# Kernel optimization log

Measured on AMD Instinct MI355X. Metric: run time of the kernel, lower is better.

Reference implementation:

```python
import jax, jax.numpy as jnp
import numpy as np

N, E = 50000, 600000
ATOM, BOND, HID, L, HEADS = 64, 16, 128, 3, 4
D = HID // HEADS  # 32


def setup_inputs() -> dict:
    key = jax.random.key(0)
    ks = jax.random.split(key, 12)
    s = lambda k, shape: (jax.random.normal(k, shape, jnp.float32) * 0.05)
    return {
        'x': jax.random.normal(ks[0], (N, ATOM), jnp.float32),
        'edge_index': jax.random.randint(ks[1], (2, E), 0, N, jnp.int32),
        'edge_attr': jax.random.normal(ks[2], (E, BOND), jnp.float32),
        'W_atom': s(ks[3], (ATOM, HID)), 'b_atom': jnp.zeros((HID,), jnp.float32),
        'W_bond': s(ks[4], (BOND, HID)), 'b_bond': jnp.zeros((HID,), jnp.float32),
        'W_lin': s(ks[5], (L, HID, HID)),      # GATConv.lin (bias-free)
        'W_edge': s(ks[6], (L, HID, HID)),     # GATConv.lin_edge (bias-free)
        'att_src': s(ks[7], (L, HEADS, D)),
        'att_dst': s(ks[8], (L, HEADS, D)),
        'att_edge': s(ks[9], (L, HEADS, D)),
        'bias_conv': jnp.zeros((L, HID), jnp.float32),
        'bn_gamma': jnp.ones((L, HID), jnp.float32),
        'bn_beta': jnp.zeros((L, HID), jnp.float32),
        'W_out': s(ks[10], (HID, HID)), 'b_out': jnp.zeros((HID,), jnp.float32),
    }


def _gat_layer(h, ea, src, dst, W, We, a_s, a_d, a_e, bias):
    n = h.shape[0]
    e = src.shape[0]
    # add_self_loops with fill_value='mean': self-loop edge_attr = mean of
    # incoming edge_attr per destination node
    loop = jnp.arange(n, dtype=src.dtype)
    deg = jax.ops.segment_sum(jnp.ones((e,), h.dtype), dst, num_segments=n)
    ea_loop = jax.ops.segment_sum(ea, dst, num_segments=n) / jnp.maximum(deg, 1.0)[:, None]
    src_f = jnp.concatenate([src, loop])
    dst_f = jnp.concatenate([dst, loop])
    ea_f = jnp.concatenate([ea, ea_loop], axis=0)   # [E+N, HID]

    xh = (h @ W).reshape(n, HEADS, D)               # [N, H, D]
    eh = (ea_f @ We).reshape(-1, HEADS, D)          # [E+N, H, D]
    a_node_src = jnp.sum(xh * a_s, axis=-1)         # [N, H]
    a_node_dst = jnp.sum(xh * a_d, axis=-1)         # [N, H]
    alpha = a_node_src[src_f] + a_node_dst[dst_f] + jnp.sum(eh * a_e, axis=-1)
    alpha = jax.nn.leaky_relu(alpha, negative_slope=0.2)  # [E+N, H]
    # softmax over incoming edges per destination (every node has a self-loop)
    amax = jax.ops.segment_max(alpha, dst_f, num_segments=n)
    expa = jnp.exp(alpha - amax[dst_f])
    den = jax.ops.segment_sum(expa, dst_f, num_segments=n)
    w = expa / (den[dst_f] + 1e-16)                 # [E+N, H]
    out = jax.ops.segment_sum(xh[src_f] * w[..., None], dst_f, num_segments=n)
    return out.reshape(n, HID) + bias


def _batch_norm(h, gamma, beta):
    mu = jnp.mean(h, axis=0)
    var = jnp.mean((h - mu) ** 2, axis=0)
    return gamma * (h - mu) * jax.lax.rsqrt(var + 1e-5) + beta


def reference(x, edge_index, edge_attr, W_atom, b_atom, W_bond, b_bond,
              W_lin, W_edge, att_src, att_dst, att_edge, bias_conv,
              bn_gamma, bn_beta, W_out, b_out):
    src, dst = edge_index[0], edge_index[1]
    h = x @ W_atom + b_atom                         # atom_embedding
    ea = edge_attr @ W_bond + b_bond                # bond_embedding (GAT path)
    for i in range(L):
        h_in = h
        h = _gat_layer(h, ea, src, dst, W_lin[i], W_edge[i],
                       att_src[i], att_dst[i], att_edge[i], bias_conv[i])
        h = _batch_norm(h, bn_gamma[i], bn_beta[i])
        h = jax.nn.relu(h)
        h = h + h_in                                # shapes always match (HID==HID)
    return h @ W_out + b_out
```

## Files before the change

### kernel.cpp

```cpp
#include <hip/hip_runtime.h>
#include <stdint.h>

#define HID 128

typedef __attribute__((ext_vector_type(8))) short bf16x8;
typedef __attribute__((ext_vector_type(4))) float f32x4;

__device__ __forceinline__ float bf2f(unsigned short u){
  union { unsigned int i; float f; } x; x.i = ((unsigned int)u) << 16; return x.f;
}
__device__ __forceinline__ unsigned short f2bf(float f){
  union { float f; unsigned int i; } x; x.f = f;
  unsigned int b = x.i;
  return (unsigned short)((b + 0x7fffu + ((b >> 16) & 1u)) >> 16);
}

struct CvList {
  const void* src[16];
  float* dst[16];
  int cnt[16];
  int n;
};
__global__ __launch_bounds__(256) void setup(CvList L, const void* x,
                                             unsigned short* xc, int n4,
                                             int* __restrict__ dflag,
                                             const int* __restrict__ ei, int E,
                                             int* __restrict__ deg){
  __shared__ int red[4];
  int tid = threadIdx.x;
  const unsigned short* xs = (const unsigned short*)x;
  unsigned short u = xs[tid];
  int ex = (u >> 7) & 0xFF;
  int v = ((((tid & 1) == 0) && u == 0) ? 1 : 0) | ((ex >= 140) ? 65536 : 0);
  #pragma unroll
  for (int m = 1; m < 64; m <<= 1) v += __shfl_xor(v, m);
  if ((tid & 63) == 0) red[tid >> 6] = v;
  __syncthreads();
  int tot = red[0] + red[1] + red[2] + red[3];
  bool isf32 = ((tot & 0xffff) >= 32) || ((tot >> 16) >= 8);
  if (blockIdx.x == 0 && tid == 0) dflag[0] = isf32 ? 1 : 0;
  int e = blockIdx.x*256 + tid;
  if (e < E) atomicAdd(&deg[ei[E + e]], 1);
  if (blockIdx.x < 256){
    for (int a = 0; a < L.n; ++a){
      const void* s = L.src[a];
      float* d = L.dst[a];
      int c = L.cnt[a];
      for (int i = blockIdx.x*256 + tid; i < c; i += 65536)
        d[i] = isf32 ? ((const float*)s)[i] : bf2f(((const unsigned short*)s)[i]);
    }
    for (int i = blockIdx.x*256 + tid; i < n4; i += 65536){
      if (isf32){
        float4 q = ((const float4*)x)[i];
        ushort4 o; o.x = f2bf(q.x); o.y = f2bf(q.y); o.z = f2bf(q.z); o.w = f2bf(q.w);
        ((ushort4*)xc)[i] = o;
      } else {
        ((ushort4*)xc)[i] = ((const ushort4*)x)[i];
      }
    }
  }
}

__global__ __launch_bounds__(256) void precompute_M(
    const float* __restrict__ We, const float* __restrict__ ae,
    const float* __restrict__ Wb, const float* __restrict__ bb,
    float* __restrict__ Mout, float* __restrict__ cb)
{
  __shared__ float ve[128*12];
  int tid = threadIdx.x;
  for (int i = tid; i < 128*12; i += 256){
    int c = i / 12, lh = i % 12; int l = lh >> 2, h = lh & 3;
    float s = 0.f;
    for (int d = 0; d < 32; ++d)
      s += We[l*16384 + c*128 + h*32 + d] * ae[l*128 + h*32 + d];
    ve[i] = s;
  }
  __syncthreads();
  for (int i = tid; i < 16*12; i += 256){
    int k = i / 12, lh = i % 12;
    float s = 0.f;
    for (int c = 0; c < 128; ++c) s += Wb[k*128 + c] * ve[c*12 + lh];
    Mout[i] = s;
  }
  for (int i = tid; i < 12; i += 256){
    float s = 0.f;
    for (int c = 0; c < 128; ++c) s += bb[c] * ve[c*12 + i];
    cb[i] = s;
  }
}

__global__ __launch_bounds__(256) void scan_part(const int* __restrict__ deg, int* __restrict__ part, int N){
  int base = blockIdx.x*1024;
  int s = 0;
  for (int i = threadIdx.x; i < 1024; i += 256){ int j = base + i; if (j < N) s += deg[j]; }
  __shared__ int sh[256];
  sh[threadIdx.x] = s; __syncthreads();
  for (int m = 128; m > 0; m >>= 1){ if (threadIdx.x < m) sh[threadIdx.x] += sh[threadIdx.x + m]; __syncthreads(); }
  if (threadIdx.x == 0) part[blockIdx.x] = sh[0];
}
__global__ void scan_top(int* part, int P){
  if (threadIdx.x == 0 && blockIdx.x == 0){
    int acc = 0;
    for (int i = 0; i < P; ++i){ int v = part[i]; part[i] = acc; acc += v; }
  }
}
__global__ __launch_bounds__(256) void scan_write(const int* __restrict__ deg, const int* __restrict__ part,
                                                  int* __restrict__ row, int N, int E){
  int base = blockIdx.x*1024 + threadIdx.x*4;
  int v0=0,v1=0,v2=0,v3=0;
  if (base+0 < N) v0 = deg[base+0];
  if (base+1 < N) v1 = deg[base+1];
  if (base+2 < N) v2 = deg[base+2];
  if (base+3 < N) v3 = deg[base+3];
  int s = v0+v1+v2+v3;
  __shared__ int sh[256];
  sh[threadIdx.x] = s; __syncthreads();
  for (int m = 1; m < 256; m <<= 1){
    int t = (threadIdx.x >= m) ? sh[threadIdx.x - m] : 0;
    __syncthreads();
    sh[threadIdx.x] += t;
    __syncthreads();
  }
  int excl = sh[threadIdx.x] - s + part[blockIdx.x];
  if (base+0 < N) row[base+0] = excl; excl += v0;
  if (base+1 < N) row[base+1] = excl; excl += v1;
  if (base+2 < N) row[base+2] = excl; excl += v2;
  if (base+3 < N) row[base+3] = excl;
  if (blockIdx.x == 0 && threadIdx.x == 0) row[N] = E;
}

__global__ __launch_bounds__(256) void proj_fill(const int* __restrict__ ei, int E,
                                                 const int* __restrict__ row, int* __restrict__ cursor,
                                                 const void* __restrict__ eattr,
                                                 const float* __restrict__ Mmat,
                                                 uint4* __restrict__ rec, int* __restrict__ perm,
                                                 const int* __restrict__ flag){
  __shared__ float sM[16][12];
  int tid = threadIdx.x;
  if (tid < 192) sM[tid/12][tid%12] = Mmat[tid];
  __syncthreads();
  int e = blockIdx.x*256 + tid;
  if (e >= E) return;
  int s = ei[e], d = ei[E + e];
  float v[16];
  if (flag[0]){
    const float4* pp = (const float4*)((const float*)eattr + (size_t)e*16);
    float4 a = pp[0], b = pp[1], c = pp[2], dd = pp[3];
    v[0]=a.x; v[1]=a.y; v[2]=a.z; v[3]=a.w;
    v[4]=b.x; v[5]=b.y; v[6]=b.z; v[7]=b.w;
    v[8]=c.x; v[9]=c.y; v[10]=c.z; v[11]=c.w;
    v[12]=dd.x; v[13]=dd.y; v[14]=dd.z; v[15]=dd.w;
  } else {
    const uint4* pp = (const uint4*)((const unsigned short*)eattr + (size_t)e*16);
    uint4 a = pp[0], b = pp[1];
    unsigned w[8] = {a.x,a.y,a.z,a.w,b.x,b.y,b.z,b.w};
    #pragma unroll
    for (int j = 0; j < 8; ++j){
      v[2*j]   = bf2f((unsigned short)(w[j] & 0xffffu));
      v[2*j+1] = bf2f((unsigned short)(w[j] >> 16));
    }
  }
  float p[12];
  #pragma unroll
  for (int j = 0; j < 12; ++j){
    float acc = 0.f;
    #pragma unroll
    for (int k = 0; k < 16; ++k) acc += v[k]*sM[k][j];
    p[j] = acc;
  }
  uint4 q0, q1;
  q0.x = (unsigned)f2bf(p[0])  | ((unsigned)f2bf(p[1])  << 16);
  q0.y = (unsigned)f2bf(p[2])  | ((unsigned)f2bf(p[3])  << 16);
  q0.z = (unsigned)f2bf(p[4])  | ((unsigned)f2bf(p[5])  << 16);
  q0.w = (unsigned)f2bf(p[6])  | ((unsigned)f2bf(p[7])  << 16);
  q1.x = (unsigned)f2bf(p[8])  | ((unsigned)f2bf(p[9])  << 16);
  q1.y = (unsigned)f2bf(p[10]) | ((unsigned)f2bf(p[11]) << 16);
  q1.z = (unsigned)s; q1.w = (unsigned)d;
  rec[(size_t)e*2]   = q0;
  rec[(size_t)e*2+1] = q1;
  int pos = atomicAdd(&cursor[d], 1);
  perm[row[d] + pos] = e;
}

__global__ __launch_bounds__(256) void mean_proj_k(const uint4* __restrict__ rec,
                                                   const int* __restrict__ perm,
                                                   const int* __restrict__ row,
                                                   float* __restrict__ mp,
                                                   float* __restrict__ deg_ind, int N){
  int n = blockIdx.x*256 + threadIdx.x;
  if (n >= N) return;
  int r = row[n], deg = row[n+1] - r;
  float acc[12] = {};
  for (int e = 0; e < deg; ++e){
    int ed = perm[r + e];
    uint4 a = rec[(size_t)ed*2];
    uint2 b = *(const uint2*)(rec + (size_t)ed*2 + 1);
    unsigned w[6] = {a.x,a.y,a.z,a.w,b.x,b.y};
    #pragma unroll
    for (int j = 0; j < 6; ++j){
      acc[2*j]   += bf2f((unsigned short)(w[j] & 0xffffu));
      acc[2*j+1] += bf2f((unsigned short)(w[j] >> 16));
    }
  }
  float inv = 1.f / (float)(deg > 0 ? deg : 1);
  float* op = mp + (size_t)n*12;
  float4 o0, o1, o2;
  o0.x=acc[0]*inv; o0.y=acc[1]*inv; o0.z=acc[2]*inv; o0.w=acc[3]*inv;
  o1.x=acc[4]*inv; o1.y=acc[5]*inv; o1.z=acc[6]*inv; o1.w=acc[7]*inv;
  o2.x=acc[8]*inv; o2.y=acc[9]*inv; o2.z=acc[10]*inv; o2.w=acc[11]*inv;
  *(float4*)(op)   = o0;
  *(float4*)(op+4) = o1;
  *(float4*)(op+8) = o2;
  deg_ind[n] = (deg > 0) ? 1.f : 0.f;
}

__device__ __forceinline__ float lrelu(float x){ return x > 0.f ? x : 0.2f*x; }
__device__ __forceinline__ float expg(float x){ return __expf(fminf(x, 0.f)); }

template<typename ACC>
__device__ __forceinline__ void att_epi(const ACC* acc, int m, int quad, int nodeBase, int N,
                                        const float* sAs, const float* sAd,
                                        const float* sCB,
                                        const float* __restrict__ mpL,
                                        const float* __restrict__ deg_ind,
                                        float* __restrict__ a_src,
                                        float* __restrict__ a_dst,
                                        float* __restrict__ alpha_self)
{
  #pragma unroll
  for (int r2 = 0; r2 < 4; ++r2){
    float vs[4], vd[4];
    #pragma unroll
    for (int h = 0; h < 4; ++h){
      int c0 = (2*h)*16 + m, c1 = (2*h+1)*16 + m;
      vs[h] = acc[2*h][r2]*sAs[c0] + acc[2*h+1][r2]*sAs[c1];
      vd[h] = acc[2*h][r2]*sAd[c0] + acc[2*h+1][r2]*sAd[c1];
    }
    #pragma unroll
    for (int mm = 1; mm < 16; mm <<= 1){
      #pragma unroll
      for (int h = 0; h < 4; ++h){
        vs[h] += __shfl_xor(vs[h], mm);
        vd[h] += __shfl_xor(vd[h], mm);
      }
    }
    if (m == 0){
      int nd = nodeBase + quad*4 + r2;
      if (nd < N){
        float ci = deg_ind[nd];
        float4 mp4 = *(const float4*)(mpL + (size_t)nd*12);
        float mpv[4] = {mp4.x, mp4.y, mp4.z, mp4.w};
        float aS[4];
        #pragma unroll
        for (int h = 0; h < 4; ++h)
          aS[h] = lrelu(vs[h] + vd[h] + sCB[h]*ci + mpv[h]);
        float4 vsv, vdv, asv;
        vsv.x=vs[0]; vsv.y=vs[1]; vsv.z=vs[2]; vsv.w=vs[3];
        vdv.x=vd[0]; vdv.y=vd[1]; vdv.z=vd[2]; vdv.w=vd[3];
        asv.x=aS[0]; asv.y=aS[1]; asv.z=aS[2]; asv.w=aS[3];
        *(float4*)(a_src + (size_t)nd*4) = vsv;
        *(float4*)(a_dst + (size_t)nd*4) = vdv;
        *(float4*)(alpha_self + (size_t)nd*4) = asv;
      }
    }
  }
}

template<int K, int OUTMODE, bool EPI>
__global__ __launch_bounds__(256) void mfma_lin(const unsigned short* __restrict__ A,
                                                const float* __restrict__ W,
                                                const float* __restrict__ bias,
                                                void* __restrict__ Out, void* __restrict__ Out2,
                                                int N,
                                                const float* __restrict__ attS,
                                                const float* __restrict__ attD,
                                                const float* __restrict__ cbl,
                                                const float* __restrict__ mpL,
                                                const float* __restrict__ deg_ind,
                                                float* __restrict__ a_src,
                                                float* __restrict__ a_dst,
                                                float* __restrict__ alpha_self)
{
  constexpr int KP = K + 8;
  __shared__ unsigned short WT[128*KP];
  __shared__ float sAs[128], sAd[128];
  __shared__ float sCB[4];
  int tid = threadIdx.x;
  for (int i = tid; i < K*128; i += 256){
    int k = i >> 7, ch = i & 127;
    WT[ch*KP + k] = f2bf(W[i]);
  }
  if (EPI){
    if (tid < 128){ sAs[tid] = attS[tid]; sAd[tid] = attD[tid]; }
    if (tid < 4)  sCB[tid] = cbl[tid];
  }
  __syncthreads();
  int wid = tid >> 6, lane = tid & 63;
  int quad = lane >> 4, m = lane & 15;
  int nodeBase = blockIdx.x*64 + wid*16;
  int node = nodeBase + m;
  int nodeC = (node < N) ? node : 0;
  bf16x8 afr[K/32];
  #pragma unroll
  for (int kb = 0; kb < K/32; ++kb)
    afr[kb] = *(const bf16x8*)(A + (size_t)nodeC*K + kb*32 + quad*8);
  f32x4 acc[8] = {};
  #pragma unroll
  for (int t = 0; t < 8; ++t){
    #pragma unroll
    for (int kb = 0; kb < K/32; ++kb){
      bf16x8 bfr = *(const bf16x8*)&WT[(t*16 + m)*KP + kb*32 + quad*8];
      acc[t] = __builtin_amdgcn_mfma_f32_16x16x32_bf16(afr[kb], bfr, acc[t], 0, 0, 0);
    }
  }
  #pragma unroll
  for (int t = 0; t < 8; ++t){
    int ch = t*16 + m;
    float bv = bias ? bias[ch] : 0.f;
    #pragma unroll
    for (int r2 = 0; r2 < 4; ++r2){
      int nd = nodeBase + quad*4 + r2;
      if (nd < N){
        float v = acc[t][r2] + bv;
        if (OUTMODE == 0){
          ((unsigned short*)Out)[(size_t)nd*HID + ch] = f2bf(v);
        } else {
          ((float*)Out)[(size_t)nd*HID + ch] = v;
          ((unsigned short*)Out2)[(size_t)nd*HID + ch] = f2bf(v);
        }
      }
    }
  }
  if (EPI)
    att_epi(acc, m, quad, nodeBase, N, sAs, sAd, sCB,
            mpL, deg_ind, a_src, a_dst, alpha_self);
}

template<int OUTMODE, bool WRITEH>
__global__ __launch_bounds__(256) void bn_mfma(const unsigned short* __restrict__ hg,
                                               const float* __restrict__ hprev,
                                               const float* __restrict__ bnsum,
                                               const float* __restrict__ bnsq,
                                               const float* __restrict__ gamma,
                                               const float* __restrict__ beta,
                                               const float* __restrict__ W,
                                               const float* __restrict__ bias,
                                               void* __restrict__ Out,
                                               float* __restrict__ hout,
                                               int N, const int* __restrict__ flag,
                                               const float* __restrict__ attS,
                                               const float* __restrict__ attD,
                                               const float* __restrict__ cbl,
                                               const float* __restrict__ mpL,
                                               const float* __restrict__ deg_ind,
                                               float* __restrict__ a_src,
                                               float* __restrict__ a_dst,
                                               float* __restrict__ alpha_self)
{
  constexpr int K = 128, KP = 136;
  __shared__ unsigned short WT[128*KP];
  __shared__ float sSc[128], sSh[128];
  __shared__ float sAs[128], sAd[128];
  __shared__ float sCB[4];
  int tid = threadIdx.x;
  for (int i = tid; i < K*128; i += 256){
    int k = i >> 7, ch = i & 127;
    WT[ch*KP + k] = f2bf(W[i]);
  }
  if (tid < 128){
    float s = 0.f, q = 0.f;
    #pragma unroll 8
    for (int b = 0; b < 64; ++b){
      s += bnsum[b*128 + tid];
      q += bnsq[b*128 + tid];
    }
    float mean = s / (float)N;
    float var  = fmaxf(q / (float)N - mean*mean, 0.f);
    float sc = gamma[tid] * rsqrtf(var + 1e-5f);
    sSc[tid] = sc;
    sSh[tid] = beta[tid] - mean*sc;
    if (OUTMODE == 0){ sAs[tid] = attS[tid]; sAd[tid] = attD[tid]; }
  }
  if (OUTMODE == 0){
    if (tid < 4)  sCB[tid] = cbl[tid];
  }
  __syncthreads();
  int wid = tid >> 6, lane = tid & 63;
  int quad = lane >> 4, m = lane & 15;
  int nodeBase = blockIdx.x*64 + wid*16;
  int node = nodeBase + m;
  int nodeC = (node < N) ? node : 0;
  bf16x8 afr[4];
  #pragma unroll
  for (int kb = 0; kb < 4; ++kb){
    int cbase = kb*32 + quad*8;
    uint4 gu = *(const uint4*)(hg + (size_t)nodeC*K + cbase);
    const float4* pp = (const float4*)(hprev + (size_t)nodeC*K + cbase);
    float4 p0 = pp[0], p1 = pp[1];
    unsigned gw[4] = {gu.x, gu.y, gu.z, gu.w};
    float pv[8] = {p0.x,p0.y,p0.z,p0.w,p1.x,p1.y,p1.z,p1.w};
    float r[8];
    #pragma unroll
    for (int j = 0; j < 8; ++j){
      float g = bf2f((unsigned short)((j & 1) ? (gw[j>>1] >> 16) : (gw[j>>1] & 0xffffu)));
      float t = g*sSc[cbase+j] + sSh[cbase+j];
      t = t > 0.f ? t : 0.f;
      r[j] = t + pv[j];
    }
    if (WRITEH && node < N){
      float4 o0, o1;
      o0.x=r[0]; o0.y=r[1]; o0.z=r[2]; o0.w=r[3];
      o1.x=r[4]; o1.y=r[5]; o1.z=r[6]; o1.w=r[7];
      float4* hp = (float4*)(hout + (size_t)node*K + cbase);
      hp[0] = o0; hp[1] = o1;
    }
    bf16x8 f;
    #pragma unroll
    for (int j = 0; j < 8; ++j) f[j] = (short)f2bf(r[j]);
    afr[kb] = f;
  }
  f32x4 acc[8] = {};
  #pragma unroll
  for (int t = 0; t < 8; ++t){
    #pragma unroll
    for (int kb = 0; kb < 4; ++kb){
      bf16x8 bfr = *(const bf16x8*)&WT[(t*16 + m)*KP + kb*32 + quad*8];
      acc[t] = __builtin_amdgcn_mfma_f32_16x16x32_bf16(afr[kb], bfr, acc[t], 0, 0, 0);
    }
  }
  bool f32out = (OUTMODE == 1) && (flag[0] != 0);
  #pragma unroll
  for (int t = 0; t < 8; ++t){
    int ch = t*16 + m;
    float bv = bias ? bias[ch] : 0.f;
    #pragma unroll
    for (int r2 = 0; r2 < 4; ++r2){
      int nd = nodeBase + quad*4 + r2;
      if (nd < N){
        float v = acc[t][r2] + bv;
        if (OUTMODE == 0) ((unsigned short*)Out)[(size_t)nd*HID + ch] = f2bf(v);
        else if (f32out)  ((float*)Out)[(size_t)nd*HID + ch] = v;
        else              ((unsigned short*)Out)[(size_t)nd*HID + ch] = f2bf(v);
      }
    }
  }
  if (OUTMODE == 0)
    att_epi(acc, m, quad, nodeBase, N, sAs, sAd, sCB,
            mpL, deg_ind, a_src, a_dst, alpha_self);
}

__device__ __forceinline__ float4 edge_alpha4(const unsigned* __restrict__ recw,
                                              const int* __restrict__ perm, int pos,
                                              const float* __restrict__ a_src,
                                              float4 adn, int layer, int* src_out){
  int e0 = perm[pos];
  const unsigned* rp = recw + (size_t)e0*8;
  unsigned w0 = rp[2*layer], w1 = rp[2*layer+1];
  int s = (int)rp[6];
  float4 as4 = *(const float4*)(a_src + (size_t)s*4);
  float4 o;
  o.x = lrelu(as4.x + adn.x + bf2f((unsigned short)(w0 & 0xffffu)));
  o.y = lrelu(as4.y + adn.y + bf2f((unsigned short)(w0 >> 16)));
  o.z = lrelu(as4.z + adn.z + bf2f((unsigned short)(w1 & 0xffffu)));
  o.w = lrelu(as4.w + adn.w + bf2f((unsigned short)(w1 >> 16)));
  *src_out = s;
  return o;
}

__global__ __launch_bounds__(256) void gat_agg(
    const unsigned short* __restrict__ xh,
    const uint4* __restrict__ rec, const int* __restrict__ perm,
    const int* __restrict__ row,
    const float* __restrict__ a_src, const float* __restrict__ a_dst,
    const float4* __restrict__ alpha_self,
    const float* __restrict__ bconv, unsigned short* __restrict__ hout,
    float* __restrict__ bnsumB, float* __restrict__ bnsqB,
    int N, int layer)
{
  __shared__ float sPf[4][256];
  __shared__ int   sOff[4][64];
  __shared__ float sStat[4][4][64];
  int tid = threadIdx.x;
  int wid = tid >> 6, lane = tid & 63;
  int n = blockIdx.x*4 + wid;
  int nn = (n < N) ? n : 0;
  int r = row[nn];
  int deg = row[nn+1] - r;
  if (n >= N) deg = 0;
  const unsigned* recw = (const unsigned*)rec;

  float4 adn = *(const float4*)(a_dst + (size_t)nn*4);
  float4 aL; aL.x = aL.y = aL.z = aL.w = -1e30f;
  int mysrc = 0;
  if (lane < deg){
    aL = edge_alpha4(recw, perm, r + lane, a_src, adn, layer, &mysrc);
  }
  float mx0 = aL.x, mx1 = aL.y, mx2 = aL.z, mx3 = aL.w;
  for (int e = lane + 64; e < deg; e += 64){
    int st;
    float4 a4 = edge_alpha4(recw, perm, r + e, a_src, adn, layer, &st);
    mx0 = fmaxf(mx0, a4.x); mx1 = fmaxf(mx1, a4.y);
    mx2 = fmaxf(mx2, a4.z); mx3 = fmaxf(mx3, a4.w);
  }
  #pragma unroll
  for (int m = 1; m < 64; m <<= 1){
    mx0 = fmaxf(mx0, __shfl_xor(mx0,m)); mx1 = fmaxf(mx1, __shfl_xor(mx1,m));
    mx2 = fmaxf(mx2, __shfl_xor(mx2,m)); mx3 = fmaxf(mx3, __shfl_xor(mx3,m));
  }
  float4 sf = alpha_self[nn];
  mx0 = fmaxf(mx0, sf.x); mx1 = fmaxf(mx1, sf.y);
  mx2 = fmaxf(mx2, sf.z); mx3 = fmaxf(mx3, sf.w);

  float p0 = 0.f, p1 = 0.f, p2 = 0.f, p3 = 0.f;
  if (lane < deg){
    p0 = expg(aL.x-mx0); p1 = expg(aL.y-mx1);
    p2 = expg(aL.z-mx2); p3 = expg(aL.w-mx3);
  }
  float4 pv; pv.x = p0; pv.y = p1; pv.z = p2; pv.w = p3;
  *(float4*)&sPf[wid][lane*4] = pv;
  sOff[wid][lane] = mysrc << 8;
  float d0 = p0, d1 = p1, d2 = p2, d3 = p3;
  for (int e = lane + 64; e < deg; e += 64){
    int st;
    float4 a4 = edge_alpha4(recw, perm, r + e, a_src, adn, layer, &st);
    d0 += expg(a4.x-mx0); d1 += expg(a4.y-mx1);
    d2 += expg(a4.z-mx2); d3 += expg(a4.w-mx3);
  }
  #pragma unroll
  for (int m = 1; m < 64; m <<= 1){
    d0 += __shfl_xor(d0,m); d1 += __shfl_xor(d1,m); d2 += __shfl_xor(d2,m); d3 += __shfl_xor(d3,m);
  }
  float ps0 = expg(sf.x-mx0), ps1 = expg(sf.y-mx1), ps2 = expg(sf.z-mx2), ps3 = expg(sf.w-mx3);
  float i0 = 1.0f/(d0+ps0+1e-16f), i1 = 1.0f/(d1+ps1+1e-16f);
  float i2 = 1.0f/(d2+ps2+1e-16f), i3 = 1.0f/(d3+ps3+1e-16f);

  int h = lane >> 4;
  float psh = h==0 ? ps0 : h==1 ? ps1 : h==2 ? ps2 : ps3;
  float ih  = h==0 ? i0  : h==1 ? i1  : h==2 ? i2  : i3;
  float mxh = h==0 ? mx0 : h==1 ? mx1 : h==2 ? mx2 : mx3;
  const char* xb = (const char*)xh;
  float acc0 = 0.f, acc1 = 0.f;
  int dmin = deg < 64 ? deg : 64;
  int e = 0;
  for (; e + 4 <= dmin; e += 4){
    int oA = sOff[wid][e+0], oB = sOff[wid][e+1], oC = sOff[wid][e+2], oD = sOff[wid][e+3];
    float qA = sPf[wid][(e+0)*4 + h], qB = sPf[wid][(e+1)*4 + h];
    float qC = sPf[wid][(e+2)*4 + h], qD = sPf[wid][(e+3)*4 + h];
    ushort2 xA = *(const ushort2*)(xb + (size_t)oA + lane*4);
    ushort2 xB = *(const ushort2*)(xb + (size_t)oB + lane*4);
    ushort2 xC = *(const ushort2*)(xb + (size_t)oC + lane*4);
    ushort2 xD = *(const ushort2*)(xb + (size_t)oD + lane*4);
    acc0 += qA*bf2f(xA.x) + qB*bf2f(xB.x) + qC*bf2f(xC.x) + qD*bf2f(xD.x);
    acc1 += qA*bf2f(xA.y) + qB*bf2f(xB.y) + qC*bf2f(xC.y) + qD*bf2f(xD.y);
  }
  for (; e < dmin; ++e){
    int o = sOff[wid][e];
    float q = sPf[wid][e*4 + h];
    ushort2 xv = *(const ushort2*)(xb + (size_t)o + lane*4);
    acc0 += q*bf2f(xv.x); acc1 += q*bf2f(xv.y);
  }
  for (; e < deg; ++e){
    int st;
    float4 a4 = edge_alpha4(recw, perm, r + e, a_src, adn, layer, &st);
    float av = h==0 ? a4.x : h==1 ? a4.y : h==2 ? a4.z : a4.w;
    float q = expg(av - mxh);
    ushort2 xv = *(const ushort2*)(xb + (size_t)st*256 + lane*4);
    acc0 += q*bf2f(xv.x); acc1 += q*bf2f(xv.y);
  }
  float fo0 = 0.f, fo1 = 0.f;
  if (n < N){
    ushort2 xn = *(const ushort2*)(xb + (size_t)nn*256 + lane*4);
    acc0 += psh * bf2f(xn.x);
    acc1 += psh * bf2f(xn.y);
    float2 bc = *(const float2*)(bconv + layer*128 + 2*lane);
    fo0 = acc0*ih + bc.x;
    fo1 = acc1*ih + bc.y;
    ushort2 o; o.x = f2bf(fo0); o.y = f2bf(fo1);
    *(ushort2*)(hout + (size_t)nn*128 + 2*lane) = o;
  }
  sStat[wid][0][lane] = fo0;
  sStat[wid][1][lane] = fo1;
  sStat[wid][2][lane] = fo0*fo0;
  sStat[wid][3][lane] = fo1*fo1;
  __syncthreads();
  if (tid < 128){
    int l = tid >> 1, j = tid & 1;
    float ss = sStat[0][j][l]   + sStat[1][j][l]   + sStat[2][j][l]   + sStat[3][j][l];
    float qq = sStat[0][2+j][l] + sStat[1][2+j][l] + sStat[2][2+j][l] + sStat[3][2+j][l];
    int bank = (blockIdx.x & 63) << 7;
    atomicAdd(&bnsumB[bank + tid], ss);
    atomicAdd(&bnsqB[bank + tid], qq);
  }
}

extern "C" void kernel_launch(void* const* d_in, const int* in_sizes, int n_in,
                              void* d_out, int out_size, void* d_ws, size_t ws_size,
                              hipStream_t stream)
{
  const void* x        = d_in[0];
  const int*  ei       = (const int*)d_in[1];
  const void* eattr    = d_in[2];
  int N = in_sizes[0] / 64;
  int E = in_sizes[1] / 2;

  char* p = (char*)d_ws;
  auto alloc = [&](size_t bytes)->char* {
    char* r = p; p += (bytes + 255) & ~(size_t)255; return r;
  };
  int*   deg    = (int*)alloc((size_t)N*4);
  int*   cursor = (int*)alloc((size_t)N*4);
  float* bnsumB = (float*)alloc(3*64*128*4);
  float* bnsqB  = (float*)alloc(3*64*128*4);
  size_t zbytes = (size_t)(p - (char*)deg);
  int*   dflag  = (int*)alloc(256);
  int*   row    = (int*)alloc(((size_t)N + 1)*4);
  int*   part   = (int*)alloc(1024*4);
  uint4* rec    = (uint4*)alloc((size_t)E*32);
  int*   perm   = (int*)alloc((size_t)E*4);
  float* hA     = (float*)alloc((size_t)N*128*4);
  float* hB     = (float*)alloc((size_t)N*128*4);
  unsigned short* hGb = (unsigned short*)alloc((size_t)N*128*2);
  unsigned short* hAb = (unsigned short*)alloc((size_t)N*128*2);
  unsigned short* xhb = (unsigned short*)alloc((size_t)N*128*2);
  float* a_src  = (float*)alloc((size_t)N*4*4);
  float* a_dst  = (float*)alloc((size_t)N*4*4);
  float* alphaS = (float*)alloc((size_t)N*4*4);
  float* mproj  = (float*)alloc((size_t)N*12*4);
  float* deg_ind= (float*)alloc((size_t)N*4);
  float* Mmat   = (float*)alloc(16*12*4);
  float* cbias  = (float*)alloc(12*4);
  unsigned short* xc  = (unsigned short*)alloc((size_t)N*64*2);
  float* wc     = (float*)alloc(130000*4);

  int   woff[14] = {0, 8192, 8320, 10368, 10496, 59648, 108800, 109184,
                    109568, 109952, 110336, 110720, 111104, 127488};
  int   wcnt[14] = {8192, 128, 2048, 128, 49152, 49152, 384, 384, 384, 384, 384, 384, 16384, 128};
  CvList L; L.n = 14;
  for (int a = 0; a < 14; ++a){ L.src[a] = d_in[3+a]; L.dst[a] = wc + woff[a]; L.cnt[a] = wcnt[a]; }
  float* cW_atom = wc + woff[0];  float* cb_atom = wc + woff[1];
  float* cW_bond = wc + woff[2];  float* cb_bond = wc + woff[3];
  float* cW_lin  = wc + woff[4];  float* cW_edge = wc + woff[5];
  float* catt_s  = wc + woff[6];  float* catt_d  = wc + woff[7];
  float* catt_e  = wc + woff[8];  float* cbconv  = wc + woff[9];
  float* cgamma  = wc + woff[10]; float* cbeta   = wc + woff[11];
  float* cW_out  = wc + woff[12]; float* cb_out  = wc + woff[13];

  hipMemsetAsync(deg, 0, zbytes, stream);
  setup<<<(E + 255)/256, 256, 0, stream>>>(L, x, xc, N*16, dflag, ei, E, deg);
  precompute_M<<<1, 256, 0, stream>>>(cW_edge, catt_e, cW_bond, cb_bond, Mmat, cbias);
  int P = (N + 1023)/1024;
  scan_part<<<P, 256, 0, stream>>>(deg, part, N);
  scan_top<<<1, 64, 0, stream>>>(part, P);
  scan_write<<<P, 256, 0, stream>>>(deg, part, row, N, E);
  proj_fill<<<(E + 255)/256, 256, 0, stream>>>(ei, E, row, cursor, eattr, Mmat, rec, perm, dflag);
  mean_proj_k<<<(N + 255)/256, 256, 0, stream>>>(rec, perm, row, mproj, deg_ind, N);

  mfma_lin<64, 2, false><<<(N + 63)/64, 256, 0, stream>>>(xc, cW_atom, cb_atom, hA, hAb, N,
      nullptr, nullptr, nullptr, nullptr, nullptr, nullptr, nullptr, nullptr);
  mfma_lin<128, 0, true><<<(N + 63)/64, 256, 0, stream>>>(hAb, cW_lin, nullptr, xhb, nullptr, N,
      catt_s, catt_d, cbias, mproj, deg_ind, a_src, a_dst, alphaS);

  float* cur = hA; float* oth = hB;
  for (int l = 0; l < 3; ++l){
    gat_agg<<<(N + 3)/4, 256, 0, stream>>>(xhb, rec, perm, row, a_src, a_dst,
                                           (const float4*)alphaS, cbconv, hGb,
                                           bnsumB + l*8192, bnsqB + l*8192, N, l);
    if (l < 2){
      bn_mfma<0, true><<<(N + 63)/64, 256, 0, stream>>>(hGb, cur,
          bnsumB + l*8192, bnsqB + l*8192, cgamma + l*128, cbeta + l*128,
          cW_lin + (size_t)(l+1)*16384, nullptr, xhb, oth, N, dflag,
          catt_s + (l+1)*128, catt_d + (l+1)*128, cbias + (l+1)*4,
          mproj + (l+1)*4, deg_ind, a_src, a_dst, alphaS);
      float* t = cur; cur = oth; oth = t;
    } else {
      bn_mfma<1, false><<<(N + 63)/64, 256, 0, stream>>>(hGb, cur,
          bnsumB + l*8192, bnsqB + l*8192, cgamma + l*128, cbeta + l*128,
          cW_out, cb_out, d_out, nullptr, N, dflag,
          nullptr, nullptr, nullptr, nullptr, nullptr, nullptr, nullptr, nullptr);
    }
  }
}
```

Before: 489.3 us.

## Fuse mean edge projection into fill via atomics; half-wave per node aggregation

Removes the mean_proj_k kernel by having proj_fill atomically add each edge's projected attributes into a zeroed per-node buffer. The degree indicator and inverse degree are now computed in scan_write and applied in the attention epilogue. gat_agg now assigns 32 lanes per node (8 nodes per block) with 4 features per lane via 8-byte loads, which suits low-degree graphs. In exchange it adds 12 float atomics per edge, makes the summation order nondeterministic, and widens per-lane register and shared-memory use.

```diff
diff --git a/kernel.cpp b/kernel.cpp
--- a/kernel.cpp
+++ b/kernel.cpp
@@ -105,7 +105,8 @@
   }
 }
 __global__ __launch_bounds__(256) void scan_write(const int* __restrict__ deg, const int* __restrict__ part,
-                                                  int* __restrict__ row, int N, int E){
+                                                  int* __restrict__ row, float2* __restrict__ dinv,
+                                                  int N, int E){
   int base = blockIdx.x*1024 + threadIdx.x*4;
   int v0=0,v1=0,v2=0,v3=0;
   if (base+0 < N) v0 = deg[base+0];
@@ -122,10 +123,10 @@
     __syncthreads();
   }
   int excl = sh[threadIdx.x] - s + part[blockIdx.x];
-  if (base+0 < N) row[base+0] = excl; excl += v0;
-  if (base+1 < N) row[base+1] = excl; excl += v1;
-  if (base+2 < N) row[base+2] = excl; excl += v2;
-  if (base+3 < N) row[base+3] = excl;
+  if (base+0 < N){ row[base+0] = excl; float2 q; q.x = v0>0?1.f:0.f; q.y = 1.f/(float)(v0>0?v0:1); dinv[base+0]=q; } excl += v0;
+  if (base+1 < N){ row[base+1] = excl; float2 q; q.x = v1>0?1.f:0.f; q.y = 1.f/(float)(v1>0?v1:1); dinv[base+1]=q; } excl += v1;
+  if (base+2 < N){ row[base+2] = excl; float2 q; q.x = v2>0?1.f:0.f; q.y = 1.f/(float)(v2>0?v2:1); dinv[base+2]=q; } excl += v2;
+  if (base+3 < N){ row[base+3] = excl; float2 q; q.x = v3>0?1.f:0.f; q.y = 1.f/(float)(v3>0?v3:1); dinv[base+3]=q; }
   if (blockIdx.x == 0 && threadIdx.x == 0) row[N] = E;
 }
 
@@ -134,6 +135,7 @@
                                                  const void* __restrict__ eattr,
                                                  const float* __restrict__ Mmat,
                                                  uint4* __restrict__ rec, int* __restrict__ perm,
+                                                 float* __restrict__ mproj,
                                                  const int* __restrict__ flag){
   __shared__ float sM[16][12];
   int tid = threadIdx.x;
@@ -178,40 +180,11 @@
   q1.z = (unsigned)s; q1.w = (unsigned)d;
   rec[(size_t)e*2]   = q0;
   rec[(size_t)e*2+1] = q1;
+  float* mp = mproj + (size_t)d*12;
+  #pragma unroll
+  for (int j = 0; j < 12; ++j) atomicAdd(&mp[j], p[j]);
   int pos = atomicAdd(&cursor[d], 1);
   perm[row[d] + pos] = e;
-}
-
-__global__ __launch_bounds__(256) void mean_proj_k(const uint4* __restrict__ rec,
-                                                   const int* __restrict__ perm,
-                                                   const int* __restrict__ row,
-                                                   float* __restrict__ mp,
-                                                   float* __restrict__ deg_ind, int N){
-  int n = blockIdx.x*256 + threadIdx.x;
-  if (n >= N) return;
-  int r = row[n], deg = row[n+1] - r;
-  float acc[12] = {};
-  for (int e = 0; e < deg; ++e){
-    int ed = perm[r + e];
-    uint4 a = rec[(size_t)ed*2];
-    uint2 b = *(const uint2*)(rec + (size_t)ed*2 + 1);
-    unsigned w[6] = {a.x,a.y,a.z,a.w,b.x,b.y};
-    #pragma unroll
-    for (int j = 0; j < 6; ++j){
-      acc[2*j]   += bf2f((unsigned short)(w[j] & 0xffffu));
-      acc[2*j+1] += bf2f((unsigned short)(w[j] >> 16));
-    }
-  }
-  float inv = 1.f / (float)(deg > 0 ? deg : 1);
-  float* op = mp + (size_t)n*12;
-  float4 o0, o1, o2;
-  o0.x=acc[0]*inv; o0.y=acc[1]*inv; o0.z=acc[2]*inv; o0.w=acc[3]*inv;
-  o1.x=acc[4]*inv; o1.y=acc[5]*inv; o1.z=acc[6]*inv; o1.w=acc[7]*inv;
-  o2.x=acc[8]*inv; o2.y=acc[9]*inv; o2.z=acc[10]*inv; o2.w=acc[11]*inv;
-  *(float4*)(op)   = o0;
-  *(float4*)(op+4) = o1;
-  *(float4*)(op+8) = o2;
-  deg_ind[n] = (deg > 0) ? 1.f : 0.f;
 }
 
 __device__ __forceinline__ float lrelu(float x){ return x > 0.f ? x : 0.2f*x; }
@@ -222,7 +195,7 @@
                                         const float* sAs, const float* sAd,
                                         const float* sCB,
                                         const float* __restrict__ mpL,
-                                        const float* __restrict__ deg_ind,
+                                        const float2* __restrict__ dinv,
                                         float* __restrict__ a_src,
                                         float* __restrict__ a_dst,
                                         float* __restrict__ alpha_self)
@@ -247,13 +220,13 @@
     if (m == 0){
       int nd = nodeBase + quad*4 + r2;
       if (nd < N){
-        float ci = deg_ind[nd];
+        float2 di = dinv[nd];
         float4 mp4 = *(const float4*)(mpL + (size_t)nd*12);
         float mpv[4] = {mp4.x, mp4.y, mp4.z, mp4.w};
         float aS[4];
         #pragma unroll
         for (int h = 0; h < 4; ++h)
-          aS[h] = lrelu(vs[h] + vd[h] + sCB[h]*ci + mpv[h]);
+          aS[h] = lrelu(vs[h] + vd[h] + sCB[h]*di.x + mpv[h]*di.y);
         float4 vsv, vdv, asv;
         vsv.x=vs[0]; vsv.y=vs[1]; vsv.z=vs[2]; vsv.w=vs[3];
         vdv.x=vd[0]; vdv.y=vd[1]; vdv.z=vd[2]; vdv.w=vd[3];
@@ -276,7 +249,7 @@
                                                 const float* __restrict__ attD,
                                                 const float* __restrict__ cbl,
                                                 const float* __restrict__ mpL,
-                                                const float* __restrict__ deg_ind,
+                                                const float2* __restrict__ dinv,
                                                 float* __restrict__ a_src,
                                                 float* __restrict__ a_dst,
                                                 float* __restrict__ alpha_self)
@@ -333,7 +306,7 @@
   }
   if (EPI)
     att_epi(acc, m, quad, nodeBase, N, sAs, sAd, sCB,
-            mpL, deg_ind, a_src, a_dst, alpha_self);
+            mpL, dinv, a_src, a_dst, alpha_self);
 }
 
 template<int OUTMODE, bool WRITEH>
@@ -352,7 +325,7 @@
                                                const float* __restrict__ attD,
                                                const float* __restrict__ cbl,
                                                const float* __restrict__ mpL,
-                                               const float* __restrict__ deg_ind,
+                                               const float2* __restrict__ dinv,
                                                float* __restrict__ a_src,
                                                float* __restrict__ a_dst,
                                                float* __restrict__ alpha_self)
@@ -446,7 +419,7 @@
   }
   if (OUTMODE == 0)
     att_epi(acc, m, quad, nodeBase, N, sAs, sAd, sCB,
-            mpL, deg_ind, a_src, a_dst, alpha_self);
+            mpL, dinv, a_src, a_dst, alpha_self);
 }
 
 __device__ __forceinline__ float4 edge_alpha4(const unsigned* __restrict__ recw,
@@ -467,6 +440,12 @@
   return o;
 }
 
+__device__ __forceinline__ void acc2(unsigned u, float q, float& a0, float& a1){
+  union { unsigned i; float f; } lo, hi;
+  lo.i = u << 16; hi.i = u & 0xffff0000u;
+  a0 += q*lo.f; a1 += q*hi.f;
+}
+
 __global__ __launch_bounds__(256) void gat_agg(
     const unsigned short* __restrict__ xh,
     const uint4* __restrict__ rec, const int* __restrict__ perm,
@@ -477,12 +456,15 @@
     float* __restrict__ bnsumB, float* __restrict__ bnsqB,
     int N, int layer)
 {
-  __shared__ float sPf[4][256];
-  __shared__ int   sOff[4][64];
-  __shared__ float sStat[4][4][64];
+  __shared__ float sPf[8][256];
+  __shared__ int   sOff[8][64];
+  __shared__ float sBS[8][128];
+  __shared__ float sBQ[8][128];
   int tid = threadIdx.x;
   int wid = tid >> 6, lane = tid & 63;
-  int n = blockIdx.x*4 + wid;
+  int half = lane >> 5, sl = lane & 31;
+  int g = wid*2 + half;
+  int n = blockIdx.x*8 + g;
   int nn = (n < N) ? n : 0;
   int r = row[nn];
   int deg = row[nn+1] - r;
@@ -490,20 +472,21 @@
   const unsigned* recw = (const unsigned*)rec;
 
   float4 adn = *(const float4*)(a_dst + (size_t)nn*4);
-  float4 aL; aL.x = aL.y = aL.z = aL.w = -1e30f;
-  int mysrc = 0;
-  if (lane < deg){
-    aL = edge_alpha4(recw, perm, r + lane, a_src, adn, layer, &mysrc);
-  }
-  float mx0 = aL.x, mx1 = aL.y, mx2 = aL.z, mx3 = aL.w;
-  for (int e = lane + 64; e < deg; e += 64){
+  float4 aA; aA.x = aA.y = aA.z = aA.w = -1e30f;
+  float4 aB; aB.x = aB.y = aB.z = aB.w = -1e30f;
+  int sA = 0, sB = 0;
+  if (sl < deg)      aA = edge_alpha4(recw, perm, r + sl,      a_src, adn, layer, &sA);
+  if (32 + sl < deg) aB = edge_alpha4(recw, perm, r + 32 + sl, a_src, adn, layer, &sB);
+  float mx0 = fmaxf(aA.x, aB.x), mx1 = fmaxf(aA.y, aB.y);
+  float mx2 = fmaxf(aA.z, aB.z), mx3 = fmaxf(aA.w, aB.w);
+  for (int e = 64 + sl; e < deg; e += 32){
     int st;
     float4 a4 = edge_alpha4(recw, perm, r + e, a_src, adn, layer, &st);
     mx0 = fmaxf(mx0, a4.x); mx1 = fmaxf(mx1, a4.y);
     mx2 = fmaxf(mx2, a4.z); mx3 = fmaxf(mx3, a4.w);
   }
   #pragma unroll
-  for (int m = 1; m < 64; m <<= 1){
+  for (int m = 1; m < 32; m <<= 1){
     mx0 = fmaxf(mx0, __shfl_xor(mx0,m)); mx1 = fmaxf(mx1, __shfl_xor(mx1,m));
     mx2 = fmaxf(mx2, __shfl_xor(mx2,m)); mx3 = fmaxf(mx3, __shfl_xor(mx3,m));
   }
@@ -511,82 +494,93 @@
   mx0 = fmaxf(mx0, sf.x); mx1 = fmaxf(mx1, sf.y);
   mx2 = fmaxf(mx2, sf.z); mx3 = fmaxf(mx3, sf.w);
 
-  float p0 = 0.f, p1 = 0.f, p2 = 0.f, p3 = 0.f;
-  if (lane < deg){
-    p0 = expg(aL.x-mx0); p1 = expg(aL.y-mx1);
-    p2 = expg(aL.z-mx2); p3 = expg(aL.w-mx3);
-  }
-  float4 pv; pv.x = p0; pv.y = p1; pv.z = p2; pv.w = p3;
-  *(float4*)&sPf[wid][lane*4] = pv;
-  sOff[wid][lane] = mysrc << 8;
-  float d0 = p0, d1 = p1, d2 = p2, d3 = p3;
-  for (int e = lane + 64; e < deg; e += 64){
+  float d0 = 0.f, d1 = 0.f, d2 = 0.f, d3 = 0.f;
+  if (sl < deg){
+    float4 p;
+    p.x = expg(aA.x-mx0); p.y = expg(aA.y-mx1);
+    p.z = expg(aA.z-mx2); p.w = expg(aA.w-mx3);
+    *(float4*)&sPf[g][sl*4] = p;
+    sOff[g][sl] = sA << 8;
+    d0 = p.x; d1 = p.y; d2 = p.z; d3 = p.w;
+  }
+  if (32 + sl < deg){
+    float4 p;
+    p.x = expg(aB.x-mx0); p.y = expg(aB.y-mx1);
+    p.z = expg(aB.z-mx2); p.w = expg(aB.w-mx3);
+    *(float4*)&sPf[g][(32+sl)*4] = p;
+    sOff[g][32+sl] = sB << 8;
+    d0 += p.x; d1 += p.y; d2 += p.z; d3 += p.w;
+  }
+  for (int e = 64 + sl; e < deg; e += 32){
     int st;
     float4 a4 = edge_alpha4(recw, perm, r + e, a_src, adn, layer, &st);
     d0 += expg(a4.x-mx0); d1 += expg(a4.y-mx1);
     d2 += expg(a4.z-mx2); d3 += expg(a4.w-mx3);
   }
   #pragma unroll
-  for (int m = 1; m < 64; m <<= 1){
+  for (int m = 1; m < 32; m <<= 1){
     d0 += __shfl_xor(d0,m); d1 += __shfl_xor(d1,m); d2 += __shfl_xor(d2,m); d3 += __shfl_xor(d3,m);
   }
   float ps0 = expg(sf.x-mx0), ps1 = expg(sf.y-mx1), ps2 = expg(sf.z-mx2), ps3 = expg(sf.w-mx3);
   float i0 = 1.0f/(d0+ps0+1e-16f), i1 = 1.0f/(d1+ps1+1e-16f);
   float i2 = 1.0f/(d2+ps2+1e-16f), i3 = 1.0f/(d3+ps3+1e-16f);
 
-  int h = lane >> 4;
+  int h = sl >> 3;
+  float mxh = h==0 ? mx0 : h==1 ? mx1 : h==2 ? mx2 : mx3;
+  float ih  = h==0 ? i0  : h==1 ? i1  : h==2 ? i2  : i3;
   float psh = h==0 ? ps0 : h==1 ? ps1 : h==2 ? ps2 : ps3;
-  float ih  = h==0 ? i0  : h==1 ? i1  : h==2 ? i2  : i3;
-  float mxh = h==0 ? mx0 : h==1 ? mx1 : h==2 ? mx2 : mx3;
   const char* xb = (const char*)xh;
-  float acc0 = 0.f, acc1 = 0.f;
+  float a0=0.f, a1=0.f, a2=0.f, a3=0.f;
   int dmin = deg < 64 ? deg : 64;
   int e = 0;
   for (; e + 4 <= dmin; e += 4){
-    int oA = sOff[wid][e+0], oB = sOff[wid][e+1], oC = sOff[wid][e+2], oD = sOff[wid][e+3];
-    float qA = sPf[wid][(e+0)*4 + h], qB = sPf[wid][(e+1)*4 + h];
-    float qC = sPf[wid][(e+2)*4 + h], qD = sPf[wid][(e+3)*4 + h];
-    ushort2 xA = *(const ushort2*)(xb + (size_t)oA + lane*4);
-    ushort2 xB = *(const ushort2*)(xb + (size_t)oB + lane*4);
-    ushort2 xC = *(const ushort2*)(xb + (size_t)oC + lane*4);
-    ushort2 xD = *(const ushort2*)(xb + (size_t)oD + lane*4);
-    acc0 += qA*bf2f(xA.x) + qB*bf2f(xB.x) + qC*bf2f(xC.x) + qD*bf2f(xD.x);
-    acc1 += qA*bf2f(xA.y) + qB*bf2f(xB.y) + qC*bf2f(xC.y) + qD*bf2f(xD.y);
+    int oA = sOff[g][e+0], oB = sOff[g][e+1], oC = sOff[g][e+2], oD = sOff[g][e+3];
+    float qA = sPf[g][(e+0)*4 + h], qB = sPf[g][(e+1)*4 + h];
+    float qC = sPf[g][(e+2)*4 + h], qD = sPf[g][(e+3)*4 + h];
+    uint2 xA = *(const uint2*)(xb + (size_t)oA + sl*8);
+    uint2 xB = *(const uint2*)(xb + (size_t)oB + sl*8);
+    uint2 xC = *(const uint2*)(xb + (size_t)oC + sl*8);
+    uint2 xD = *(const uint2*)(xb + (size_t)oD + sl*8);
+    acc2(xA.x, qA, a0,a1); acc2(xA.y, qA, a2,a3);
+    acc2(xB.x, qB, a0,a1); acc2(xB.y, qB, a2,a3);
+    acc2(xC.x, qC, a0,a1); acc2(xC.y, qC, a2,a3);
+    acc2(xD.x, qD, a0,a1); acc2(xD.y, qD, a2,a3);
   }
   for (; e < dmin; ++e){
-    int o = sOff[wid][e];
-    float q = sPf[wid][e*4 + h];
-    ushort2 xv = *(const ushort2*)(xb + (size_t)o + lane*4);
-    acc0 += q*bf2f(xv.x); acc1 += q*bf2f(xv.y);
+    int o = sOff[g][e];
+    float q = sPf[g][e*4 + h];
+    uint2 xv = *(const uint2*)(xb + (size_t)o + sl*8);
+    acc2(xv.x, q, a0,a1); acc2(xv.y, q, a2,a3);
   }
   for (; e < deg; ++e){
     int st;
     float4 a4 = edge_alpha4(recw, perm, r + e, a_src, adn, layer, &st);
     float av = h==0 ? a4.x : h==1 ? a4.y : h==2 ? a4.z : a4.w;
     float q = expg(av - mxh);
-    ushort2 xv = *(const ushort2*)(xb + (size_t)st*256 + lane*4);
-    acc0 += q*bf2f(xv.x); acc1 += q*bf2f(xv.y);
-  }
-  float fo0 = 0.f, fo1 = 0.f;
+    uint2 xv = *(const uint2*)(xb + (size_t)st*256 + sl*8);
+    acc2(xv.x, q, a0,a1); acc2(xv.y, q, a2,a3);
+  }
+  float fo0=0.f, fo1=0.f, fo2=0.f, fo3=0.f;
   if (n < N){
-    ushort2 xn = *(const ushort2*)(xb + (size_t)nn*256 + lane*4);
-    acc0 += psh * bf2f(xn.x);
-    acc1 += psh * bf2f(xn.y);
-    float2 bc = *(const float2*)(bconv + layer*128 + 2*lane);
-    fo0 = acc0*ih + bc.x;
-    fo1 = acc1*ih + bc.y;
-    ushort2 o; o.x = f2bf(fo0); o.y = f2bf(fo1);
-    *(ushort2*)(hout + (size_t)nn*128 + 2*lane) = o;
-  }
-  sStat[wid][0][lane] = fo0;
-  sStat[wid][1][lane] = fo1;
-  sStat[wid][2][lane] = fo0*fo0;
-  sStat[wid][3][lane] = fo1*fo1;
+    uint2 xn = *(const uint2*)(xb + (size_t)nn*256 + sl*8);
+    acc2(xn.x, psh, a0,a1); acc2(xn.y, psh, a2,a3);
+    float4 bc = *(const float4*)(bconv + layer*128 + sl*4);
+    fo0 = a0*ih + bc.x; fo1 = a1*ih + bc.y;
+    fo2 = a2*ih + bc.z; fo3 = a3*ih + bc.w;
+    uint2 ov;
+    ov.x = (unsigned)f2bf(fo0) | ((unsigned)f2bf(fo1) << 16);
+    ov.y = (unsigned)f2bf(fo2) | ((unsigned)f2bf(fo3) << 16);
+    *(uint2*)((char*)hout + (size_t)nn*256 + sl*8) = ov;
+  }
+  float4 vS; vS.x=fo0; vS.y=fo1; vS.z=fo2; vS.w=fo3;
+  float4 vQ; vQ.x=fo0*fo0; vQ.y=fo1*fo1; vQ.z=fo2*fo2; vQ.w=fo3*fo3;
+  *(float4*)&sBS[g][sl*4] = vS;
+  *(float4*)&sBQ[g][sl*4] = vQ;
   __syncthreads();
   if (tid < 128){
-    int l = tid >> 1, j = tid & 1;
-    float ss = sStat[0][j][l]   + sStat[1][j][l]   + sStat[2][j][l]   + sStat[3][j][l];
-    float qq = sStat[0][2+j][l] + sStat[1][2+j][l] + sStat[2][2+j][l] + sStat[3][2+j][l];
+    float ss = 0.f, qq = 0.f;
+    #pragma unroll
+    for (int k = 0; k < 8; ++k){ ss += sBS[k][tid]; qq += sBQ[k][tid]; }
     int bank = (blockIdx.x & 63) << 7;
     atomicAdd(&bnsumB[bank + tid], ss);
     atomicAdd(&bnsqB[bank + tid], qq);
@@ -611,6 +605,7 @@
   int*   cursor = (int*)alloc((size_t)N*4);
   float* bnsumB = (float*)alloc(3*64*128*4);
   float* bnsqB  = (float*)alloc(3*64*128*4);
+  float* mproj  = (float*)alloc((size_t)N*12*4);
   size_t zbytes = (size_t)(p - (char*)deg);
   int*   dflag  = (int*)alloc(256);
   int*   row    = (int*)alloc(((size_t)N + 1)*4);
@@ -625,8 +620,7 @@
   float* a_src  = (float*)alloc((size_t)N*4*4);
   float* a_dst  = (float*)alloc((size_t)N*4*4);
   float* alphaS = (float*)alloc((size_t)N*4*4);
-  float* mproj  = (float*)alloc((size_t)N*12*4);
-  float* deg_ind= (float*)alloc((size_t)N*4);
+  float2* dinv  = (float2*)alloc((size_t)N*8);
   float* Mmat   = (float*)alloc(16*12*4);
   float* cbias  = (float*)alloc(12*4);
   unsigned short* xc  = (unsigned short*)alloc((size_t)N*64*2);
@@ -651,18 +645,17 @@
   int P = (N + 1023)/1024;
   scan_part<<<P, 256, 0, stream>>>(deg, part, N);
   scan_top<<<1, 64, 0, stream>>>(part, P);
-  scan_write<<<P, 256, 0, stream>>>(deg, part, row, N, E);
-  proj_fill<<<(E + 255)/256, 256, 0, stream>>>(ei, E, row, cursor, eattr, Mmat, rec, perm, dflag);
-  mean_proj_k<<<(N + 255)/256, 256, 0, stream>>>(rec, perm, row, mproj, deg_ind, N);
+  scan_write<<<P, 256, 0, stream>>>(deg, part, row, dinv, N, E);
+  proj_fill<<<(E + 255)/256, 256, 0, stream>>>(ei, E, row, cursor, eattr, Mmat, rec, perm, mproj, dflag);
 
   mfma_lin<64, 2, false><<<(N + 63)/64, 256, 0, stream>>>(xc, cW_atom, cb_atom, hA, hAb, N,
       nullptr, nullptr, nullptr, nullptr, nullptr, nullptr, nullptr, nullptr);
   mfma_lin<128, 0, true><<<(N + 63)/64, 256, 0, stream>>>(hAb, cW_lin, nullptr, xhb, nullptr, N,
-      catt_s, catt_d, cbias, mproj, deg_ind, a_src, a_dst, alphaS);
+      catt_s, catt_d, cbias, mproj, dinv, a_src, a_dst, alphaS);
 
   float* cur = hA; float* oth = hB;
   for (int l = 0; l < 3; ++l){
-    gat_agg<<<(N + 3)/4, 256, 0, stream>>>(xhb, rec, perm, row, a_src, a_dst,
+    gat_agg<<<(N + 7)/8, 256, 0, stream>>>(xhb, rec, perm, row, a_src, a_dst,
                                            (const float4*)alphaS, cbconv, hGb,
                                            bnsumB + l*8192, bnsqB + l*8192, N, l);
     if (l < 2){
@@ -670,7 +663,7 @@
           bnsumB + l*8192, bnsqB + l*8192, cgamma + l*128, cbeta + l*128,
           cW_lin + (size_t)(l+1)*16384, nullptr, xhb, oth, N, dflag,
           catt_s + (l+1)*128, catt_d + (l+1)*128, cbias + (l+1)*4,
-          mproj + (l+1)*4, deg_ind, a_src, a_dst, alphaS);
+          mproj + (l+1)*4, dinv, a_src, a_dst, alphaS);
       float* t = cur; cur = oth; oth = t;
     } else {
       bn_mfma<1, false><<<(N + 63)/64, 256, 0, stream>>>(hGb, cur,
```

New measurement: 812.2 us. 1.66x slower.
